# Performance work log

Measured on AMD Instinct MI355X. Metric: run time of the kernel, lower is better.

Reference implementation:

```python
import jax, jax.numpy as jnp
import numpy as np

DIM = 512
HEADS = 8
DIM_HEAD = 64
INNER = HEADS * DIM_HEAD


def setup_inputs() -> dict:
    key = jax.random.key(0)
    k1, k2, k3, k4 = jax.random.split(key, 4)
    x = jax.random.normal(k1, (8, 2048, DIM), dtype=jnp.float32)
    # nn.Linear(dim, inner*3, bias=False): store as [dim, 3*inner] for x @ W
    w_qkv = jax.random.normal(k2, (DIM, 3 * INNER), dtype=jnp.float32) * (DIM ** -0.5)
    w_out = jax.random.normal(k3, (INNER, DIM), dtype=jnp.float32) * (INNER ** -0.5)
    b_out = jax.random.normal(k4, (DIM,), dtype=jnp.float32) * 0.01
    # learnable log-scale, init = log(dim_head**-0.5)
    log_scale = jnp.asarray(np.log(DIM_HEAD ** -0.5), dtype=jnp.float32)
    return {"x": x, "w_qkv": w_qkv, "w_out": w_out, "b_out": b_out, "log_scale": log_scale}


def reference(x, w_qkv, w_out, b_out, log_scale):
    b, n, _ = x.shape
    qkv = x @ w_qkv                                   # [b, n, 3*inner]
    q, k, v = jnp.split(qkv, 3, axis=-1)
    def to_heads(t):
        return t.reshape(b, n, HEADS, DIM_HEAD).transpose(0, 2, 1, 3)  # [b,h,n,d]
    q, k, v = to_heads(q), to_heads(k), to_heads(v)
    dots = jnp.einsum('bhid,bhjd->bhij', q, k) * jnp.exp(log_scale)    # [b,h,n,n]
    mask_value = -jnp.finfo(dots.dtype).max
    eye = jnp.eye(n, dtype=bool)
    dots = jnp.where(eye, mask_value, dots)           # exclude self token
    attn = jax.nn.softmax(dots, axis=-1)
    out = jnp.einsum('bhij,bhjd->bhid', attn, v)      # [b,h,n,d]
    out = out.transpose(0, 2, 1, 3).reshape(b, n, INNER)
    return out @ w_out + b_out
```

## Files before the change

kernel.cpp:

```cpp
#include <hip/hip_runtime.h>
#include <hip/hip_bf16.h>
#include <cstddef>

#define DIMK 512
#define HEADS 8
#define DHEAD 64
#define NSEQ 2048
#define NB 8
#define M_TOT (NB * NSEQ)

typedef __attribute__((ext_vector_type(8))) short bf16x8;
typedef __attribute__((ext_vector_type(4))) float f32x4;

__device__ __forceinline__ unsigned short f2bf(float f) {
    union { float f; unsigned int u; } v; v.f = f;
    unsigned int r = v.u + 0x7fffu + ((v.u >> 16) & 1u);
    return (unsigned short)(r >> 16);
}

__device__ __forceinline__ unsigned int pk_bf_trunc(float hi, float lo) {
    union { float f; unsigned int u; } a, b; a.f = hi; b.f = lo;
    return __builtin_amdgcn_perm(a.u, b.u, 0x07060302u);
}

__device__ __forceinline__ float fexp2(float x) {
#if __has_builtin(__builtin_amdgcn_exp2f)
    return __builtin_amdgcn_exp2f(x);
#else
    return __expf(x * 0.69314718056f);
#endif
}

__device__ __forceinline__ void glds16(const unsigned short* g, unsigned short* l) {
    __builtin_amdgcn_global_load_lds(
        (const __attribute__((address_space(1))) void*)g,
        (__attribute__((address_space(3))) void*)l, 16, 0, 0);
}

__global__ __launch_bounds__(256) void f32_to_bf16(
    const float* __restrict__ in, unsigned short* __restrict__ out)
{
    const size_t i = ((size_t)blockIdx.x * 256 + threadIdx.x) * 8;
    const float4 a = *(const float4*)(in + i);
    const float4 b = *(const float4*)(in + i + 4);
    bf16x8 o;
    o[0] = (short)f2bf(a.x); o[1] = (short)f2bf(a.y);
    o[2] = (short)f2bf(a.z); o[3] = (short)f2bf(a.w);
    o[4] = (short)f2bf(b.x); o[5] = (short)f2bf(b.y);
    o[6] = (short)f2bf(b.z); o[7] = (short)f2bf(b.w);
    *(bf16x8*)(out + i) = o;
}

__global__ __launch_bounds__(256) void transpose_both(
    const float* __restrict__ w_qkv, const float* __restrict__ w_out,
    unsigned short* __restrict__ WqT, unsigned short* __restrict__ WoT,
    const float* __restrict__ log_scale)
{
    __shared__ float t[32][33];
    const int tx = threadIdx.x & 31, ty = threadIdx.x >> 5;
    const int k0 = blockIdx.y * 32;
    const float* W; unsigned short* WT; int N, n0;
    float sc = 1.0f;
    if (blockIdx.x < 48) {
        W = w_qkv; WT = WqT; N = 1536; n0 = blockIdx.x * 32;
        if (n0 < 512) sc = __expf(log_scale[0]) * 1.4426950408889634f;
    } else {
        W = w_out; WT = WoT; N = 512; n0 = (blockIdx.x - 48) * 32;
    }
    #pragma unroll
    for (int s = 0; s < 32; s += 8)
        t[ty + s][tx] = W[(size_t)(k0 + ty + s) * N + n0 + tx];
    __syncthreads();
    #pragma unroll
    for (int s = 0; s < 32; s += 8)
        WT[(size_t)(n0 + ty + s) * DIMK + k0 + tx] = f2bf(t[tx][ty + s] * sc);
}

__global__ __launch_bounds__(256) void gemm_qkv_mfma(
    const unsigned short* __restrict__ Xb, const unsigned short* __restrict__ WT,
    unsigned short* __restrict__ Qb, unsigned short* __restrict__ Kb,
    unsigned short* __restrict__ VTb)
{
    __shared__ unsigned short As[128 * 32];
    __shared__ unsigned short Bs[128 * 32];
    const int tid = threadIdx.x, wave = tid >> 6, lane = tid & 63;
    const int l16 = lane & 15, quad = lane >> 4;
    const int m0 = blockIdx.x * 128;
    const int cb = blockIdx.y;
    const int col0 = cb * 128;
    const int wrow = wave >> 1, wcol = wave & 1;

    unsigned short* lA0 = As + (wave * 16) * 32;
    unsigned short* lA1 = As + (64 + wave * 16) * 32;
    unsigned short* lB0 = Bs + (wave * 16) * 32;
    unsigned short* lB1 = Bs + (64 + wave * 16) * 32;
    const unsigned short* gA = Xb + (size_t)(m0 + wave * 16 + (lane >> 2)) * DIMK + (lane & 3) * 8;
    const unsigned short* gB = WT + (size_t)(col0 + wave * 16 + (lane >> 2)) * DIMK + (lane & 3) * 8;

    f32x4 acc[4][4];
    #pragma unroll
    for (int i = 0; i < 4; ++i)
        #pragma unroll
        for (int j = 0; j < 4; ++j) acc[i][j] = (f32x4){0.f, 0.f, 0.f, 0.f};

    for (int k0 = 0; k0 < DIMK; k0 += 32) {
        __syncthreads();
        glds16(gA + k0, lA0);
        glds16(gA + (size_t)64 * DIMK + k0, lA1);
        glds16(gB + k0, lB0);
        glds16(gB + (size_t)64 * DIMK + k0, lB1);
        __syncthreads();
        bf16x8 af[4], bfr[4];
        #pragma unroll
        for (int i = 0; i < 4; ++i)
            af[i] = *(const bf16x8*)(As + (wrow * 64 + i * 16 + l16) * 32 + quad * 8);
        #pragma unroll
        for (int j = 0; j < 4; ++j)
            bfr[j] = *(const bf16x8*)(Bs + (wcol * 64 + j * 16 + l16) * 32 + quad * 8);
        #pragma unroll
        for (int i = 0; i < 4; ++i)
            #pragma unroll
            for (int j = 0; j < 4; ++j)
                acc[i][j] = __builtin_amdgcn_mfma_f32_16x16x32_bf16(af[i], bfr[j], acc[i][j], 0, 0, 0);
    }

    const int which = cb >> 2;
    #pragma unroll
    for (int i = 0; i < 4; ++i) {
        #pragma unroll
        for (int r = 0; r < 4; ++r) {
            const int gr = m0 + wrow * 64 + i * 16 + quad * 4 + r;
            const int bb = gr >> 11, n = gr & 2047;
            #pragma unroll
            for (int j = 0; j < 4; ++j) {
                const int col = col0 + wcol * 64 + j * 16 + l16;
                const int w = col & 511, h = w >> 6, d = w & 63;
                const size_t bh = (size_t)(bb * HEADS + h);
                const unsigned short val = f2bf(acc[i][j][r]);
                if (which == 0)      Qb[(bh * NSEQ + n) * DHEAD + d] = val;
                else if (which == 1) Kb[(bh * NSEQ + n) * DHEAD + d] = val;
                else                 VTb[(bh * DHEAD + d) * NSEQ + n] = val;
            }
        }
    }
}

__global__ __launch_bounds__(256) void gemm_out_mfma(
    const unsigned short* __restrict__ Ab, const unsigned short* __restrict__ BT,
    const float* __restrict__ bias, float* __restrict__ C)
{
    __shared__ unsigned short As[128 * 32];
    __shared__ unsigned short Bs[128 * 32];
    const int tid = threadIdx.x, wave = tid >> 6, lane = tid & 63;
    const int l16 = lane & 15, quad = lane >> 4;
    const int m0 = blockIdx.x * 128, col0 = blockIdx.y * 128;
    const int wrow = wave >> 1, wcol = wave & 1;

    unsigned short* lA0 = As + (wave * 16) * 32;
    unsigned short* lA1 = As + (64 + wave * 16) * 32;
    unsigned short* lB0 = Bs + (wave * 16) * 32;
    unsigned short* lB1 = Bs + (64 + wave * 16) * 32;
    const unsigned short* gA = Ab + (size_t)(m0 + wave * 16 + (lane >> 2)) * DIMK + (lane & 3) * 8;
    const unsigned short* gB = BT + (size_t)(col0 + wave * 16 + (lane >> 2)) * DIMK + (lane & 3) * 8;

    f32x4 acc[4][4];
    #pragma unroll
    for (int i = 0; i < 4; ++i)
        #pragma unroll
        for (int j = 0; j < 4; ++j) acc[i][j] = (f32x4){0.f, 0.f, 0.f, 0.f};

    for (int k0 = 0; k0 < DIMK; k0 += 32) {
        __syncthreads();
        glds16(gA + k0, lA0);
        glds16(gA + (size_t)64 * DIMK + k0, lA1);
        glds16(gB + k0, lB0);
        glds16(gB + (size_t)64 * DIMK + k0, lB1);
        __syncthreads();
        bf16x8 af[4], bfr[4];
        #pragma unroll
        for (int i = 0; i < 4; ++i)
            af[i] = *(const bf16x8*)(As + (wrow * 64 + i * 16 + l16) * 32 + quad * 8);
        #pragma unroll
        for (int j = 0; j < 4; ++j)
            bfr[j] = *(const bf16x8*)(Bs + (wcol * 64 + j * 16 + l16) * 32 + quad * 8);
        #pragma unroll
        for (int i = 0; i < 4; ++i)
            #pragma unroll
            for (int j = 0; j < 4; ++j)
                acc[i][j] = __builtin_amdgcn_mfma_f32_16x16x32_bf16(af[i], bfr[j], acc[i][j], 0, 0, 0);
    }

    #pragma unroll
    for (int i = 0; i < 4; ++i) {
        #pragma unroll
        for (int r = 0; r < 4; ++r) {
            const int gr = m0 + wrow * 64 + i * 16 + quad * 4 + r;
            #pragma unroll
            for (int j = 0; j < 4; ++j) {
                const int col = col0 + wcol * 64 + j * 16 + l16;
                C[(size_t)gr * 512 + col] = acc[i][j][r] + bias[col];
            }
        }
    }
}

__global__ __launch_bounds__(256) void attn_mfma(
    const unsigned short* __restrict__ Qb, const unsigned short* __restrict__ Kb,
    const unsigned short* __restrict__ VTb, unsigned short* __restrict__ O)
{
    __shared__ unsigned short Ks0[2][64 * 32];
    __shared__ unsigned short Ks1[2][64 * 32];
    __shared__ unsigned short VsA[2][64 * 32];
    __shared__ unsigned short VsB[2][64 * 32];
    __shared__ __align__(16) unsigned short Pq[4][2][16][72];

    const int tid  = threadIdx.x;
    const int wave = tid >> 6;
    const int lane = tid & 63;
    const int l16  = lane & 15;
    const int quad = lane >> 4;
    const int bh   = blockIdx.x;
    const int q0   = blockIdx.y * 128;
    const int qwA  = q0 + wave * 16;
    const int qwB  = q0 + 64 + wave * 16;

    const unsigned short* Qg = Qb  + (size_t)bh * NSEQ * DHEAD;
    const unsigned short* Kg = Kb  + (size_t)bh * NSEQ * DHEAD;
    const unsigned short* Vg = VTb + (size_t)bh * DHEAD * NSEQ;

    const bf16x8 b_qA0 = *(const bf16x8*)(Qg + (size_t)(qwA + l16) * DHEAD + quad * 8);
    const bf16x8 b_qA1 = *(const bf16x8*)(Qg + (size_t)(qwA + l16) * DHEAD + 32 + quad * 8);
    const bf16x8 b_qB0 = *(const bf16x8*)(Qg + (size_t)(qwB + l16) * DHEAD + quad * 8);
    const bf16x8 b_qB1 = *(const bf16x8*)(Qg + (size_t)(qwB + l16) * DHEAD + 32 + quad * 8);

    bf16x8 a_ones;
    #pragma unroll
    for (int i = 0; i < 8; ++i) a_ones[i] = (short)0x3F80;

    const int r16 = lane >> 2;
    const int c8  = (lane & 3) * 8;
    const unsigned short* gsrc;
    size_t rstep;
    size_t istep;
    unsigned short* db[2];
    if (wave == 0) {
        gsrc = Kg + (size_t)r16 * DHEAD + c8;
        rstep = (size_t)16 * DHEAD;  istep = (size_t)64 * DHEAD;
        db[0] = &Ks0[0][0];  db[1] = &Ks0[1][0];
    } else if (wave == 1) {
        gsrc = Kg + (size_t)r16 * DHEAD + 32 + c8;
        rstep = (size_t)16 * DHEAD;  istep = (size_t)64 * DHEAD;
        db[0] = &Ks1[0][0];  db[1] = &Ks1[1][0];
    } else if (wave == 2) {
        gsrc = Vg + (size_t)r16 * NSEQ + c8;
        rstep = (size_t)16 * NSEQ;   istep = 64;
        db[0] = &VsA[0][0];  db[1] = &VsA[1][0];
    } else {
        gsrc = Vg + (size_t)r16 * NSEQ + 32 + c8;
        rstep = (size_t)16 * NSEQ;   istep = 64;
        db[0] = &VsB[0][0];  db[1] = &VsB[1][0];
    }

    f32x4 oA[4], oB[4], laccA, laccB;
    #pragma unroll
    for (int t = 0; t < 4; ++t) { oA[t] = (f32x4){0.f,0.f,0.f,0.f}; oB[t] = (f32x4){0.f,0.f,0.f,0.f}; }
    laccA = (f32x4){0.f,0.f,0.f,0.f};
    laccB = (f32x4){0.f,0.f,0.f,0.f};

    {
        unsigned short* d0 = db[0];
        glds16(gsrc,             d0);
        glds16(gsrc +     rstep, d0 + 512);
        glds16(gsrc + 2 * rstep, d0 + 1024);
        glds16(gsrc + 3 * rstep, d0 + 1536);
        gsrc += istep;
    }

    #pragma unroll 2
    for (int it = 0; it < NSEQ / 64; ++it) {
        const int cur = it & 1;
        const int j0  = it * 64;
        __syncthreads();

        if (it < NSEQ / 64 - 1) {
            unsigned short* dn = db[cur ^ 1];
            glds16(gsrc,             dn);
            glds16(gsrc +     rstep, dn + 512);
            glds16(gsrc + 2 * rstep, dn + 1024);
            glds16(gsrc + 3 * rstep, dn + 1536);
            gsrc += istep;
        }

        float pA[4][4], pB[4][4];
        #pragma unroll
        for (int t = 0; t < 4; ++t) {
            const bf16x8 a0 = *(const bf16x8*)(&Ks0[cur][(t * 16 + l16) * 32 + quad * 8]);
            const bf16x8 a1 = *(const bf16x8*)(&Ks1[cur][(t * 16 + l16) * 32 + quad * 8]);
            f32x4 sA = (f32x4){0.f,0.f,0.f,0.f}, sB = (f32x4){0.f,0.f,0.f,0.f};
            sA = __builtin_amdgcn_mfma_f32_16x16x32_bf16(a0, b_qA0, sA, 0, 0, 0);
            sA = __builtin_amdgcn_mfma_f32_16x16x32_bf16(a1, b_qA1, sA, 0, 0, 0);
            sB = __builtin_amdgcn_mfma_f32_16x16x32_bf16(a0, b_qB0, sB, 0, 0, 0);
            sB = __builtin_amdgcn_mfma_f32_16x16x32_bf16(a1, b_qB1, sB, 0, 0, 0);
            #pragma unroll
            for (int r = 0; r < 4; ++r) { pA[t][r] = fexp2(sA[r]); pB[t][r] = fexp2(sB[r]); }
            if (j0 + 16 * t == qwA) {
                #pragma unroll
                for (int r = 0; r < 4; ++r) if (l16 == quad * 4 + r) pA[t][r] = 0.f;
            }
            if (j0 + 16 * t == qwB) {
                #pragma unroll
                for (int r = 0; r < 4; ++r) if (l16 == quad * 4 + r) pB[t][r] = 0.f;
            }
        }

        #pragma unroll
        for (int t = 0; t < 4; ++t) {
            uint2 wA, wB;
            wA.x = pk_bf_trunc(pA[t][1], pA[t][0]); wA.y = pk_bf_trunc(pA[t][3], pA[t][2]);
            wB.x = pk_bf_trunc(pB[t][1], pB[t][0]); wB.y = pk_bf_trunc(pB[t][3], pB[t][2]);
            *(uint2*)(&Pq[wave][0][l16][t * 16 + quad * 4]) = wA;
            *(uint2*)(&Pq[wave][1][l16][t * 16 + quad * 4]) = wB;
        }
        __builtin_amdgcn_wave_barrier();

        const bf16x8 b_pA0 = *(const bf16x8*)(&Pq[wave][0][l16][quad * 8]);
        const bf16x8 b_pA1 = *(const bf16x8*)(&Pq[wave][0][l16][32 + quad * 8]);
        const bf16x8 b_pB0 = *(const bf16x8*)(&Pq[wave][1][l16][quad * 8]);
        const bf16x8 b_pB1 = *(const bf16x8*)(&Pq[wave][1][l16][32 + quad * 8]);

        laccA = __builtin_amdgcn_mfma_f32_16x16x32_bf16(a_ones, b_pA0, laccA, 0, 0, 0);
        laccA = __builtin_amdgcn_mfma_f32_16x16x32_bf16(a_ones, b_pA1, laccA, 0, 0, 0);
        laccB = __builtin_amdgcn_mfma_f32_16x16x32_bf16(a_ones, b_pB0, laccB, 0, 0, 0);
        laccB = __builtin_amdgcn_mfma_f32_16x16x32_bf16(a_ones, b_pB1, laccB, 0, 0, 0);
        #pragma unroll
        for (int t = 0; t < 4; ++t) {
            const bf16x8 vA = *(const bf16x8*)(&VsA[cur][(t * 16 + l16) * 32 + quad * 8]);
            const bf16x8 vB = *(const bf16x8*)(&VsB[cur][(t * 16 + l16) * 32 + quad * 8]);
            oA[t] = __builtin_amdgcn_mfma_f32_16x16x32_bf16(vA, b_pA0, oA[t], 0, 0, 0);
            oA[t] = __builtin_amdgcn_mfma_f32_16x16x32_bf16(vB, b_pA1, oA[t], 0, 0, 0);
            oB[t] = __builtin_amdgcn_mfma_f32_16x16x32_bf16(vA, b_pB0, oB[t], 0, 0, 0);
            oB[t] = __builtin_amdgcn_mfma_f32_16x16x32_bf16(vB, b_pB1, oB[t], 0, 0, 0);
        }
    }

    const float invA = 1.0f / laccA[0];
    const float invB = 1.0f / laccB[0];
    const int bb = bh >> 3, h = bh & 7;
    {
        const int n = qwA + l16;
        unsigned short* Orow = O + ((size_t)(bb * NSEQ + n)) * 512 + h * 64;
        #pragma unroll
        for (int t = 0; t < 4; ++t) {
            ushort4 o4;
            o4.x = f2bf(oA[t][0] * invA); o4.y = f2bf(oA[t][1] * invA);
            o4.z = f2bf(oA[t][2] * invA); o4.w = f2bf(oA[t][3] * invA);
            *(ushort4*)(Orow + t * 16 + quad * 4) = o4;
        }
    }
    {
        const int n = qwB + l16;
        unsigned short* Orow = O + ((size_t)(bb * NSEQ + n)) * 512 + h * 64;
        #pragma unroll
        for (int t = 0; t < 4; ++t) {
            ushort4 o4;
            o4.x = f2bf(oB[t][0] * invB); o4.y = f2bf(oB[t][1] * invB);
            o4.z = f2bf(oB[t][2] * invB); o4.w = f2bf(oB[t][3] * invB);
            *(ushort4*)(Orow + t * 16 + quad * 4) = o4;
        }
    }
}

extern "C" void kernel_launch(void* const* d_in, const int* in_sizes, int n_in,
                              void* d_out, int out_size, void* d_ws, size_t ws_size,
                              hipStream_t stream) {
    const float* x         = (const float*)d_in[0];
    const float* w_qkv     = (const float*)d_in[1];
    const float* w_out     = (const float*)d_in[2];
    const float* b_out     = (const float*)d_in[3];
    const float* log_scale = (const float*)d_in[4];
    float* out = (float*)d_out;

    char* ws = (char*)d_ws;
    const size_t NQKV = (size_t)NB * HEADS * NSEQ * DHEAD;
    unsigned short* xb  = (unsigned short*)(ws);
    unsigned short* Qb  = (unsigned short*)(ws + 2 * NQKV);
    unsigned short* Kb  = (unsigned short*)(ws + 4 * NQKV);
    unsigned short* VTb = (unsigned short*)(ws + 6 * NQKV);
    unsigned short* Ofb = (unsigned short*)(ws + 8 * NQKV);
    unsigned short* WqT = (unsigned short*)(ws + 10 * NQKV);
    unsigned short* WoT = (unsigned short*)(ws + 10 * NQKV + 4 * 1024 * 1024);

    f32_to_bf16<<<M_TOT * DIMK / (256 * 8), 256, 0, stream>>>(x, xb);
    transpose_both<<<dim3(64, 16), 256, 0, stream>>>(w_qkv, w_out, WqT, WoT, log_scale);

    gemm_qkv_mfma<<<dim3(M_TOT / 128, 1536 / 128), 256, 0, stream>>>(xb, WqT, Qb, Kb, VTb);

    attn_mfma<<<dim3(NB * HEADS, NSEQ / 128), 256, 0, stream>>>(Qb, Kb, VTb, Ofb);

    gemm_out_mfma<<<dim3(M_TOT / 128, 512 / 128), 256, 0, stream>>>(Ofb, WoT, b_out, out);
}
```

Measured before the change: 249.9 us.

## Widen attention query tile to 256 rows and stage V-transpose through LDS

The attention kernel now gives each block 256 query rows, four 16-row groups per wave, so every K/V tile loaded into LDS serves twice as many queries and global K/V traffic is halved. The QKV GEMM epilogue for the V slice now transposes the accumulator tile in shared memory and writes VT with 16-byte coalesced stores, replacing scattered 2-byte stores. In exchange the attention kernel uses more registers and LDS and launches half as many blocks (512), which may lower occupancy and leave some CUs underused.

```diff
diff --git a/kernel.cpp b/kernel.cpp
--- a/kernel.cpp
+++ b/kernel.cpp
@@ -81,8 +81,9 @@
     unsigned short* __restrict__ Qb, unsigned short* __restrict__ Kb,
     unsigned short* __restrict__ VTb)
 {
-    __shared__ unsigned short As[128 * 32];
-    __shared__ unsigned short Bs[128 * 32];
+    __shared__ __align__(16) unsigned short pool[128 * 136];
+    unsigned short* As = pool;
+    unsigned short* Bs = pool + 4096;
     const int tid = threadIdx.x, wave = tid >> 6, lane = tid & 63;
     const int l16 = lane & 15, quad = lane >> 4;
     const int m0 = blockIdx.x * 128;
@@ -125,21 +126,51 @@
     }
 
     const int which = cb >> 2;
-    #pragma unroll
-    for (int i = 0; i < 4; ++i) {
-        #pragma unroll
-        for (int r = 0; r < 4; ++r) {
-            const int gr = m0 + wrow * 64 + i * 16 + quad * 4 + r;
-            const int bb = gr >> 11, n = gr & 2047;
+    if (which == 2) {
+        __syncthreads();
+        #pragma unroll
+        for (int i = 0; i < 4; ++i) {
             #pragma unroll
             for (int j = 0; j < 4; ++j) {
-                const int col = col0 + wcol * 64 + j * 16 + l16;
-                const int w = col & 511, h = w >> 6, d = w & 63;
-                const size_t bh = (size_t)(bb * HEADS + h);
-                const unsigned short val = f2bf(acc[i][j][r]);
-                if (which == 0)      Qb[(bh * NSEQ + n) * DHEAD + d] = val;
-                else if (which == 1) Kb[(bh * NSEQ + n) * DHEAD + d] = val;
-                else                 VTb[(bh * DHEAD + d) * NSEQ + n] = val;
+                const int c  = wcol * 64 + j * 16 + l16;
+                const int n0 = wrow * 64 + i * 16 + quad * 4;
+                uint2 w;
+                w.x = (unsigned int)f2bf(acc[i][j][0]) | ((unsigned int)f2bf(acc[i][j][1]) << 16);
+                w.y = (unsigned int)f2bf(acc[i][j][2]) | ((unsigned int)f2bf(acc[i][j][3]) << 16);
+                *(uint2*)(&pool[c * 136 + n0]) = w;
+            }
+        }
+        __syncthreads();
+        const int cbase = tid >> 4;
+        const int ln16  = tid & 15;
+        const int n0g   = m0 & 2047;
+        const int bb    = m0 >> 11;
+        const int w0    = col0 & 511;
+        #pragma unroll
+        for (int pass = 0; pass < 8; ++pass) {
+            const int cc = pass * 16 + cbase;
+            const int w  = w0 + cc;
+            const int h  = w >> 6, d = w & 63;
+            const size_t bh = (size_t)(bb * HEADS + h);
+            const bf16x8 val = *(const bf16x8*)(&pool[cc * 136 + ln16 * 8]);
+            *(bf16x8*)(VTb + (bh * DHEAD + d) * NSEQ + n0g + ln16 * 8) = val;
+        }
+    } else {
+        #pragma unroll
+        for (int i = 0; i < 4; ++i) {
+            #pragma unroll
+            for (int r = 0; r < 4; ++r) {
+                const int gr = m0 + wrow * 64 + i * 16 + quad * 4 + r;
+                const int bb = gr >> 11, n = gr & 2047;
+                #pragma unroll
+                for (int j = 0; j < 4; ++j) {
+                    const int col = col0 + wcol * 64 + j * 16 + l16;
+                    const int w = col & 511, h = w >> 6, d = w & 63;
+                    const size_t bh = (size_t)(bb * HEADS + h);
+                    const unsigned short val = f2bf(acc[i][j][r]);
+                    if (which == 0) Qb[(bh * NSEQ + n) * DHEAD + d] = val;
+                    else            Kb[(bh * NSEQ + n) * DHEAD + d] = val;
+                }
             }
         }
     }
@@ -212,7 +243,7 @@
     __shared__ unsigned short Ks1[2][64 * 32];
     __shared__ unsigned short VsA[2][64 * 32];
     __shared__ unsigned short VsB[2][64 * 32];
-    __shared__ __align__(16) unsigned short Pq[4][2][16][72];
+    __shared__ __align__(16) unsigned short Pq[4][4][16][72];
 
     const int tid  = threadIdx.x;
     const int wave = tid >> 6;
@@ -220,18 +251,23 @@
     const int l16  = lane & 15;
     const int quad = lane >> 4;
     const int bh   = blockIdx.x;
-    const int q0   = blockIdx.y * 128;
-    const int qwA  = q0 + wave * 16;
-    const int qwB  = q0 + 64 + wave * 16;
+    const int q0   = blockIdx.y * 256;
+
+    int qw[4];
+    #pragma unroll
+    for (int g = 0; g < 4; ++g) qw[g] = q0 + g * 64 + wave * 16;
 
     const unsigned short* Qg = Qb  + (size_t)bh * NSEQ * DHEAD;
     const unsigned short* Kg = Kb  + (size_t)bh * NSEQ * DHEAD;
     const unsigned short* Vg = VTb + (size_t)bh * DHEAD * NSEQ;
 
-    const bf16x8 b_qA0 = *(const bf16x8*)(Qg + (size_t)(qwA + l16) * DHEAD + quad * 8);
-    const bf16x8 b_qA1 = *(const bf16x8*)(Qg + (size_t)(qwA + l16) * DHEAD + 32 + quad * 8);
-    const bf16x8 b_qB0 = *(const bf16x8*)(Qg + (size_t)(qwB + l16) * DHEAD + quad * 8);
-    const bf16x8 b_qB1 = *(const bf16x8*)(Qg + (size_t)(qwB + l16) * DHEAD + 32 + quad * 8);
+    bf16x8 bq[4][2];
+    #pragma unroll
+    for (int g = 0; g < 4; ++g) {
+        const unsigned short* qrow = Qg + (size_t)(qw[g] + l16) * DHEAD;
+        bq[g][0] = *(const bf16x8*)(qrow + quad * 8);
+        bq[g][1] = *(const bf16x8*)(qrow + 32 + quad * 8);
+    }
 
     bf16x8 a_ones;
     #pragma unroll
@@ -261,11 +297,13 @@
         db[0] = &VsB[0][0];  db[1] = &VsB[1][0];
     }
 
-    f32x4 oA[4], oB[4], laccA, laccB;
-    #pragma unroll
-    for (int t = 0; t < 4; ++t) { oA[t] = (f32x4){0.f,0.f,0.f,0.f}; oB[t] = (f32x4){0.f,0.f,0.f,0.f}; }
-    laccA = (f32x4){0.f,0.f,0.f,0.f};
-    laccB = (f32x4){0.f,0.f,0.f,0.f};
+    f32x4 o[4][4], lacc[4];
+    #pragma unroll
+    for (int g = 0; g < 4; ++g) {
+        lacc[g] = (f32x4){0.f,0.f,0.f,0.f};
+        #pragma unroll
+        for (int t = 0; t < 4; ++t) o[g][t] = (f32x4){0.f,0.f,0.f,0.f};
+    }
 
     {
         unsigned short* d0 = db[0];
@@ -291,80 +329,68 @@
             gsrc += istep;
         }
 
-        float pA[4][4], pB[4][4];
         #pragma unroll
         for (int t = 0; t < 4; ++t) {
             const bf16x8 a0 = *(const bf16x8*)(&Ks0[cur][(t * 16 + l16) * 32 + quad * 8]);
             const bf16x8 a1 = *(const bf16x8*)(&Ks1[cur][(t * 16 + l16) * 32 + quad * 8]);
-            f32x4 sA = (f32x4){0.f,0.f,0.f,0.f}, sB = (f32x4){0.f,0.f,0.f,0.f};
-            sA = __builtin_amdgcn_mfma_f32_16x16x32_bf16(a0, b_qA0, sA, 0, 0, 0);
-            sA = __builtin_amdgcn_mfma_f32_16x16x32_bf16(a1, b_qA1, sA, 0, 0, 0);
-            sB = __builtin_amdgcn_mfma_f32_16x16x32_bf16(a0, b_qB0, sB, 0, 0, 0);
-            sB = __builtin_amdgcn_mfma_f32_16x16x32_bf16(a1, b_qB1, sB, 0, 0, 0);
-            #pragma unroll
-            for (int r = 0; r < 4; ++r) { pA[t][r] = fexp2(sA[r]); pB[t][r] = fexp2(sB[r]); }
-            if (j0 + 16 * t == qwA) {
+            float p[4][4];
+            #pragma unroll
+            for (int g = 0; g < 4; ++g) {
+                f32x4 s = (f32x4){0.f,0.f,0.f,0.f};
+                s = __builtin_amdgcn_mfma_f32_16x16x32_bf16(a0, bq[g][0], s, 0, 0, 0);
+                s = __builtin_amdgcn_mfma_f32_16x16x32_bf16(a1, bq[g][1], s, 0, 0, 0);
                 #pragma unroll
-                for (int r = 0; r < 4; ++r) if (l16 == quad * 4 + r) pA[t][r] = 0.f;
-            }
-            if (j0 + 16 * t == qwB) {
-                #pragma unroll
-                for (int r = 0; r < 4; ++r) if (l16 == quad * 4 + r) pB[t][r] = 0.f;
-            }
-        }
-
-        #pragma unroll
-        for (int t = 0; t < 4; ++t) {
-            uint2 wA, wB;
-            wA.x = pk_bf_trunc(pA[t][1], pA[t][0]); wA.y = pk_bf_trunc(pA[t][3], pA[t][2]);
-            wB.x = pk_bf_trunc(pB[t][1], pB[t][0]); wB.y = pk_bf_trunc(pB[t][3], pB[t][2]);
-            *(uint2*)(&Pq[wave][0][l16][t * 16 + quad * 4]) = wA;
-            *(uint2*)(&Pq[wave][1][l16][t * 16 + quad * 4]) = wB;
+                for (int r = 0; r < 4; ++r) p[g][r] = fexp2(s[r]);
+                if (j0 + 16 * t == qw[g]) {
+                    #pragma unroll
+                    for (int r = 0; r < 4; ++r) if (l16 == quad * 4 + r) p[g][r] = 0.f;
+                }
+            }
+            #pragma unroll
+            for (int g = 0; g < 4; ++g) {
+                uint2 w;
+                w.x = pk_bf_trunc(p[g][1], p[g][0]);
+                w.y = pk_bf_trunc(p[g][3], p[g][2]);
+                *(uint2*)(&Pq[wave][g][l16][t * 16 + quad * 4]) = w;
+            }
         }
         __builtin_amdgcn_wave_barrier();
 
-        const bf16x8 b_pA0 = *(const bf16x8*)(&Pq[wave][0][l16][quad * 8]);
-        const bf16x8 b_pA1 = *(const bf16x8*)(&Pq[wave][0][l16][32 + quad * 8]);
-        const bf16x8 b_pB0 = *(const bf16x8*)(&Pq[wave][1][l16][quad * 8]);
-        const bf16x8 b_pB1 = *(const bf16x8*)(&Pq[wave][1][l16][32 + quad * 8]);
-
-        laccA = __builtin_amdgcn_mfma_f32_16x16x32_bf16(a_ones, b_pA0, laccA, 0, 0, 0);
-        laccA = __builtin_amdgcn_mfma_f32_16x16x32_bf16(a_ones, b_pA1, laccA, 0, 0, 0);
-        laccB = __builtin_amdgcn_mfma_f32_16x16x32_bf16(a_ones, b_pB0, laccB, 0, 0, 0);
-        laccB = __builtin_amdgcn_mfma_f32_16x16x32_bf16(a_ones, b_pB1, laccB, 0, 0, 0);
+        bf16x8 bp[4][2];
+        #pragma unroll
+        for (int g = 0; g < 4; ++g) {
+            bp[g][0] = *(const bf16x8*)(&Pq[wave][g][l16][quad * 8]);
+            bp[g][1] = *(const bf16x8*)(&Pq[wave][g][l16][32 + quad * 8]);
+        }
+
+        #pragma unroll
+        for (int g = 0; g < 4; ++g) {
+            lacc[g] = __builtin_amdgcn_mfma_f32_16x16x32_bf16(a_ones, bp[g][0], lacc[g], 0, 0, 0);
+            lacc[g] = __builtin_amdgcn_mfma_f32_16x16x32_bf16(a_ones, bp[g][1], lacc[g], 0, 0, 0);
+        }
         #pragma unroll
         for (int t = 0; t < 4; ++t) {
             const bf16x8 vA = *(const bf16x8*)(&VsA[cur][(t * 16 + l16) * 32 + quad * 8]);
             const bf16x8 vB = *(const bf16x8*)(&VsB[cur][(t * 16 + l16) * 32 + quad * 8]);
-            oA[t] = __builtin_amdgcn_mfma_f32_16x16x32_bf16(vA, b_pA0, oA[t], 0, 0, 0);
-            oA[t] = __builtin_amdgcn_mfma_f32_16x16x32_bf16(vB, b_pA1, oA[t], 0, 0, 0);
-            oB[t] = __builtin_amdgcn_mfma_f32_16x16x32_bf16(vA, b_pB0, oB[t], 0, 0, 0);
-            oB[t] = __builtin_amdgcn_mfma_f32_16x16x32_bf16(vB, b_pB1, oB[t], 0, 0, 0);
-        }
-    }
-
-    const float invA = 1.0f / laccA[0];
-    const float invB = 1.0f / laccB[0];
+            #pragma unroll
+            for (int g = 0; g < 4; ++g) {
+                o[g][t] = __builtin_amdgcn_mfma_f32_16x16x32_bf16(vA, bp[g][0], o[g][t], 0, 0, 0);
+                o[g][t] = __builtin_amdgcn_mfma_f32_16x16x32_bf16(vB, bp[g][1], o[g][t], 0, 0, 0);
+            }
+        }
+    }
+
     const int bb = bh >> 3, h = bh & 7;
-    {
-        const int n = qwA + l16;
+    #pragma unroll
+    for (int g = 0; g < 4; ++g) {
+        const float inv = 1.0f / lacc[g][0];
+        const int n = qw[g] + l16;
         unsigned short* Orow = O + ((size_t)(bb * NSEQ + n)) * 512 + h * 64;
         #pragma unroll
         for (int t = 0; t < 4; ++t) {
             ushort4 o4;
-            o4.x = f2bf(oA[t][0] * invA); o4.y = f2bf(oA[t][1] * invA);
-            o4.z = f2bf(oA[t][2] * invA); o4.w = f2bf(oA[t][3] * invA);
-            *(ushort4*)(Orow + t * 16 + quad * 4) = o4;
-        }
-    }
-    {
-        const int n = qwB + l16;
-        unsigned short* Orow = O + ((size_t)(bb * NSEQ + n)) * 512 + h * 64;
-        #pragma unroll
-        for (int t = 0; t < 4; ++t) {
-            ushort4 o4;
-            o4.x = f2bf(oB[t][0] * invB); o4.y = f2bf(oB[t][1] * invB);
-            o4.z = f2bf(oB[t][2] * invB); o4.w = f2bf(oB[t][3] * invB);
+            o4.x = f2bf(o[g][t][0] * inv); o4.y = f2bf(o[g][t][1] * inv);
+            o4.z = f2bf(o[g][t][2] * inv); o4.w = f2bf(o[g][t][3] * inv);
             *(ushort4*)(Orow + t * 16 + quad * 4) = o4;
         }
     }
@@ -395,7 +421,7 @@
 
     gemm_qkv_mfma<<<dim3(M_TOT / 128, 1536 / 128), 256, 0, stream>>>(xb, WqT, Qb, Kb, VTb);
 
-    attn_mfma<<<dim3(NB * HEADS, NSEQ / 128), 256, 0, stream>>>(Qb, Kb, VTb, Ofb);
+    attn_mfma<<<dim3(NB * HEADS, NSEQ / 256), 256, 0, stream>>>(Qb, Kb, VTb, Ofb);
 
     gemm_out_mfma<<<dim3(M_TOT / 128, 512 / 128), 256, 0, stream>>>(Ofb, WoT, b_out, out);
 }
```

After: 268.7 us. 7.5% more time.
